# Performance work log

Measured on AMD Instinct MI355X. Metric: run time of the kernel, lower is better.

The kernel has to match this reference:

```python
import jax, jax.numpy as jnp
import numpy as np

EPS = 1e-08

SOBEL_X = jnp.array([[1, 0, -1], [2, 0, -2], [1, 0, -1]], dtype=jnp.float32).reshape(1, 1, 3, 3)
SOBEL_Y = jnp.array([[1, 2, 1], [0, 0, 0], [-1, -2, -1]], dtype=jnp.float32).reshape(1, 1, 3, 3)


def _conv3x3(x, k):
    # x: (B,1,H,W), k: (1,1,3,3) OIHW, padding=1 -> same spatial size
    return jax.lax.conv_general_dilated(
        x, k, window_strides=(1, 1), padding=((1, 1), (1, 1)),
        dimension_numbers=("NCHW", "OIHW", "NCHW"))


def setup_inputs() -> dict:
    key = jax.random.key(0)
    k1, k2 = jax.random.split(key)
    B, H, W = 4, 64, 64
    depth_pred = jax.random.normal(k1, (B, 1, H, W), dtype=jnp.float32)
    boundary_gt = jax.random.uniform(k2, (B, 1, H, W), dtype=jnp.float32)
    return {"depth_pred": depth_pred, "boundary_gt": boundary_gt}


def reference(depth_pred, boundary_gt):
    # Sobel gradient magnitude
    gx = _conv3x3(depth_pred, SOBEL_X)
    gy = _conv3x3(depth_pred, SOBEL_Y)
    g_depth = jnp.sqrt(gx * gx + gy * gy + EPS)

    B = depth_pred.shape[0]
    gf = g_depth.reshape(B, -1)        # (B, N)
    bf = boundary_gt.reshape(B, -1)    # (B, N)

    # Pairwise |g_i - b_j|: (B, N, N). dist1 = min over j; dist2 = min over i
    # (same matrix transposed, so build it once).
    d = jnp.abs(gf[:, :, None] - bf[:, None, :])
    dist1 = jnp.min(d, axis=2)  # (B, N) min over boundary points
    dist2 = jnp.min(d, axis=1)  # (B, N) min over gradient points
    return dist1.mean() + dist2.mean()
```

## Files before the change

kernel.cpp:

```cpp
#include <hip/hip_runtime.h>
#include <math.h>


#define N_PIX 4096
#define BLK   256
#define CHUNKS_PER_IMG 16

__device__ __forceinline__ float sobel_g(const float* __restrict__ d, int pix) {
    const int y = pix >> 6;
    const int x = pix & 63;
    const float a00 = (y > 0 && x > 0)  ? d[(y - 1) * 64 + (x - 1)] : 0.f;
    const float a01 = (y > 0)           ? d[(y - 1) * 64 + x]       : 0.f;
    const float a02 = (y > 0 && x < 63) ? d[(y - 1) * 64 + (x + 1)] : 0.f;
    const float a10 = (x > 0)           ? d[y * 64 + (x - 1)]       : 0.f;
    const float a12 = (x < 63)          ? d[y * 64 + (x + 1)]       : 0.f;
    const float a20 = (y < 63 && x > 0) ? d[(y + 1) * 64 + (x - 1)] : 0.f;
    const float a21 = (y < 63)          ? d[(y + 1) * 64 + x]       : 0.f;
    const float a22 = (y < 63 && x < 63)? d[(y + 1) * 64 + (x + 1)] : 0.f;
    const float gx = (a00 - a02) + 2.f * (a10 - a12) + (a20 - a22);
    const float gy = (a00 + 2.f * a01 + a02) - (a20 + 2.f * a21 + a22);
    return sqrtf(gx * gx + gy * gy + 1e-8f);
}

__global__ __launch_bounds__(BLK) void chamfer_kernel(
    const float* __restrict__ depth, const float* __restrict__ bnd,
    float* __restrict__ out, int blocks_per_dir, int inv_count_bits ,
    float inv_count)
{
    __shared__ float refs[N_PIX];
    __shared__ float bsum;

    const int tid = threadIdx.x;
    const int bx  = blockIdx.x;
    const int dir = (bx >= blocks_per_dir) ? 1 : 0;
    const int rem = dir ? (bx - blocks_per_dir) : bx;
    const int batch = rem >> 4;
    const int chunk = rem & (CHUNKS_PER_IMG - 1);

    const float* __restrict__ db = depth + batch * N_PIX;
    const float* __restrict__ bb = bnd   + batch * N_PIX;

    if (tid == 0) bsum = 0.f;

    if (dir == 0) {
        const float4* __restrict__ b4 = (const float4*)bb;
        float4* r4 = (float4*)refs;
        #pragma unroll
        for (int j = 0; j < (N_PIX / 4) / BLK; ++j)
            r4[tid + j * BLK] = b4[tid + j * BLK];
    } else {
        #pragma unroll
        for (int j = 0; j < N_PIX / BLK; ++j) {
            const int p = tid + j * BLK;
            refs[p] = sobel_g(db, p);
        }
    }
    __syncthreads();

    const int pix = chunk * BLK + tid;
    const float p = (dir == 0) ? sobel_g(db, pix) : bb[pix];

    float m0 = 1e30f, m1 = 1e30f, m2 = 1e30f, m3 = 1e30f;
    const float4* __restrict__ r4 = (const float4*)refs;
    #pragma unroll 8
    for (int j = 0; j < N_PIX / 4; ++j) {
        const float4 r = r4[j];
        m0 = fminf(m0, fabsf(p - r.x));
        m1 = fminf(m1, fabsf(p - r.y));
        m2 = fminf(m2, fabsf(p - r.z));
        m3 = fminf(m3, fabsf(p - r.w));
    }
    float m = fminf(fminf(m0, m1), fminf(m2, m3));

    #pragma unroll
    for (int o = 32; o > 0; o >>= 1) m += __shfl_down(m, o);
    if ((tid & 63) == 0) atomicAdd(&bsum, m);
    __syncthreads();
    if (tid == 0) atomicAdd(out, bsum * inv_count);
}

extern "C" void kernel_launch(void* const* d_in, const int* in_sizes, int n_in,
                              void* d_out, int out_size, void* d_ws, size_t ws_size,
                              hipStream_t stream) {
    const float* depth = (const float*)d_in[0];
    const float* bnd   = (const float*)d_in[1];
    float* out = (float*)d_out;

    const int B = in_sizes[0] / N_PIX;
    const int blocks_per_dir = B * CHUNKS_PER_IMG;
    const int grid = 2 * blocks_per_dir;
    const float inv_count = 1.0f / (float)(B * N_PIX);

    hipMemsetAsync(out, 0, sizeof(float), stream);
    hipLaunchKernelGGL(chamfer_kernel, dim3(grid), dim3(BLK), 0, stream,
                       depth, bnd, out, blocks_per_dir, 0, inv_count);
}
```

Measured before the change: 82.99 us.

## Precompute Sobel magnitudes in a separate kernel and read references from global memory

Adds a first kernel that computes the Sobel gradient magnitude for every pixel into workspace and zeroes the output, which replaces the memset. The chamfer kernel no longer stages the 4096 reference values in LDS. Each thread reads them directly from global memory as uniform float4 loads, using two min accumulators instead of four. This removes the redundant per-block Sobel recomputation and the LDS fill, at the cost of an extra launch and a reference stream served from cache instead of LDS.

```diff
diff --git a/kernel.cpp b/kernel.cpp
--- a/kernel.cpp
+++ b/kernel.cpp
@@ -22,12 +22,21 @@
     return sqrtf(gx * gx + gy * gy + 1e-8f);
 }
 
+__global__ __launch_bounds__(BLK) void sobel_all_kernel(
+    const float* __restrict__ depth, float* __restrict__ g_ws,
+    float* __restrict__ out)
+{
+    const int gid = blockIdx.x * BLK + threadIdx.x;
+    const int batch = gid >> 12;
+    const int pix   = gid & (N_PIX - 1);
+    g_ws[gid] = sobel_g(depth + batch * N_PIX, pix);
+    if (gid == 0) out[0] = 0.f;
+}
+
 __global__ __launch_bounds__(BLK) void chamfer_kernel(
-    const float* __restrict__ depth, const float* __restrict__ bnd,
-    float* __restrict__ out, int blocks_per_dir, int inv_count_bits ,
-    float inv_count)
+    const float* __restrict__ g_ws, const float* __restrict__ bnd,
+    float* __restrict__ out, int blocks_per_dir, float inv_count)
 {
-    __shared__ float refs[N_PIX];
     __shared__ float bsum;
 
     const int tid = threadIdx.x;
@@ -37,40 +46,24 @@
     const int batch = rem >> 4;
     const int chunk = rem & (CHUNKS_PER_IMG - 1);
 
-    const float* __restrict__ db = depth + batch * N_PIX;
-    const float* __restrict__ bb = bnd   + batch * N_PIX;
+    const float* __restrict__ gb = g_ws + batch * N_PIX;
+    const float* __restrict__ bb = bnd  + batch * N_PIX;
 
     if (tid == 0) bsum = 0.f;
-
-    if (dir == 0) {
-        const float4* __restrict__ b4 = (const float4*)bb;
-        float4* r4 = (float4*)refs;
-        #pragma unroll
-        for (int j = 0; j < (N_PIX / 4) / BLK; ++j)
-            r4[tid + j * BLK] = b4[tid + j * BLK];
-    } else {
-        #pragma unroll
-        for (int j = 0; j < N_PIX / BLK; ++j) {
-            const int p = tid + j * BLK;
-            refs[p] = sobel_g(db, p);
-        }
-    }
     __syncthreads();
 
     const int pix = chunk * BLK + tid;
-    const float p = (dir == 0) ? sobel_g(db, pix) : bb[pix];
+    const float q = dir ? bb[pix] : gb[pix];
+    const float4* __restrict__ ref4 = (const float4*)(dir ? gb : bb);
 
-    float m0 = 1e30f, m1 = 1e30f, m2 = 1e30f, m3 = 1e30f;
-    const float4* __restrict__ r4 = (const float4*)refs;
+    float m0 = 1e30f, m1 = 1e30f;
     #pragma unroll 8
     for (int j = 0; j < N_PIX / 4; ++j) {
-        const float4 r = r4[j];
-        m0 = fminf(m0, fabsf(p - r.x));
-        m1 = fminf(m1, fabsf(p - r.y));
-        m2 = fminf(m2, fabsf(p - r.z));
-        m3 = fminf(m3, fabsf(p - r.w));
+        const float4 r = ref4[j];
+        m0 = fminf(fminf(m0, fabsf(q - r.x)), fabsf(q - r.y));
+        m1 = fminf(fminf(m1, fabsf(q - r.z)), fabsf(q - r.w));
     }
-    float m = fminf(fminf(m0, m1), fminf(m2, m3));
+    float m = fminf(m0, m1);
 
     #pragma unroll
     for (int o = 32; o > 0; o >>= 1) m += __shfl_down(m, o);
@@ -84,14 +77,15 @@
                               hipStream_t stream) {
     const float* depth = (const float*)d_in[0];
     const float* bnd   = (const float*)d_in[1];
-    float* out = (float*)d_out;
+    float* out  = (float*)d_out;
+    float* g_ws = (float*)d_ws;
 
     const int B = in_sizes[0] / N_PIX;
     const int blocks_per_dir = B * CHUNKS_PER_IMG;
-    const int grid = 2 * blocks_per_dir;
     const float inv_count = 1.0f / (float)(B * N_PIX);
 
-    hipMemsetAsync(out, 0, sizeof(float), stream);
-    hipLaunchKernelGGL(chamfer_kernel, dim3(grid), dim3(BLK), 0, stream,
-                       depth, bnd, out, blocks_per_dir, 0, inv_count);
+    hipLaunchKernelGGL(sobel_all_kernel, dim3(B * N_PIX / BLK), dim3(BLK), 0,
+                       stream, depth, g_ws, out);
+    hipLaunchKernelGGL(chamfer_kernel, dim3(2 * blocks_per_dir), dim3(BLK), 0,
+                       stream, g_ws, bnd, out, blocks_per_dir, inv_count);
 }
```

After: 102.4 us. 1.23x slower.
